# Performance work log

Hardware: AMD Instinct MI355X
Metric: run time of the kernel (lower is better)

Reference implementation:

```python
import jax, jax.numpy as jnp
import numpy as np

B, SECL, WORDL = 16, 8, 512
S = SECL * WORDL
H, E, V, NOOV = 256, 128, 50000, 32
EOS = 3
FSIZE = 2  # config.mode == 'train'


def setup_inputs() -> dict:
    key = jax.random.key(0)
    ks = jax.random.split(key, 24)
    g = lambda i, shape, s=0.02: jax.random.normal(ks[i], shape, jnp.float32) * s
    inp = jax.random.randint(ks[0], (B,), 0, V)
    inp = inp.at[:4].set(EOS)  # exercise focus-update branch
    h = g(1, (B, H), 0.1)
    c = g(2, (B, H), 0.1)
    enc_outputs = g(3, (B, S, 2 * H), 1.0)
    enc_feature = g(4, (B, S, 2 * H), 0.1)
    enc_sec_output = g(5, (B, SECL, 2 * H), 1.0)
    enc_mask = jnp.ones((B, S), jnp.float32)
    sec_mask = jnp.ones((B, SECL), jnp.float32)
    prev_context = g(6, (B, 2 * H), 0.1)
    zeros_oov = jnp.zeros((B, NOOV), jnp.float32)
    enc_input_oov = jax.random.randint(ks[7], (B, S), 0, V + NOOV)
    coverage = jnp.zeros((B, S), jnp.float32)
    # sparse nonneg focus distribution over sections (guaranteed >=1 nonzero/row)
    u = jax.random.uniform(ks[8], (B, SECL))
    f = u * (u > 0.5)
    fb = jax.nn.one_hot(jnp.argmax(u, axis=1), SECL)
    f = jnp.where(f.sum(1, keepdims=True) > 0, f, fb)
    focus = f / f.sum(1, keepdims=True)
    params = dict(
        embedding=g(9, (V, E)),
        W_comb=g(10, (E, 2 * H + E)), b_comb=jnp.zeros((E,), jnp.float32),
        W_ih=g(11, (4 * H, E)), W_hh=g(12, (4 * H, H)),
        b_ih=jnp.zeros((4 * H,), jnp.float32), b_hh=jnp.zeros((4 * H,), jnp.float32),
        W_d=g(13, (2 * H, 2 * H)), b_d=jnp.zeros((2 * H,), jnp.float32),
        W_feat=g(14, (2 * H, 2 * H)), v_sec=g(15, (2 * H,)),
        W_dec=g(16, (2 * H, 2 * H)), b_dec=jnp.zeros((2 * H,), jnp.float32),
        w_cov=g(17, (2 * H,)), v_att=g(18, (2 * H,)),
        W_pgen=g(19, (1, 4 * H + E)), b_pgen=jnp.zeros((1,), jnp.float32),
        W_out=g(20, (V, 3 * H)), b_out=g(21, (V,)),
    )
    return dict(inp=inp, h=h, c=c, enc_outputs=enc_outputs, enc_feature=enc_feature,
                enc_sec_output=enc_sec_output, enc_mask=enc_mask, sec_mask=sec_mask,
                prev_context=prev_context, zeros_oov=zeros_oov, enc_input_oov=enc_input_oov,
                coverage=coverage, focus=focus, **params)


def _focus_update(focus, sad):
    # rem_mask: positions from the first nonzero of focus onward
    fz = jnp.cumprod((focus == 0).astype(sad.dtype), axis=1)
    rem_mask = (fz == 0).astype(sad.dtype)
    focus_index = jnp.sum(fz, axis=1).astype(jnp.int32)  # index of first nonzero
    focus_mask = jax.nn.one_hot(focus_index, SECL, dtype=sad.dtype)
    rem_ex = rem_mask - focus_mask
    focus_beta = sad * focus_mask
    rem_beta = sad * rem_ex
    max_rem_beta = rem_beta.max(axis=1)
    max_rem_ind = jnp.argmax(rem_beta, axis=1)
    compare = (focus_beta.max(axis=1) * 2 > max_rem_beta).astype(sad.dtype)[:, None]
    # train branch
    src = (max_rem_beta != 0).astype(sad.dtype)[:, None]
    max_rem_mask = jax.nn.one_hot(max_rem_ind, SECL, dtype=sad.dtype) * src
    cp2 = jnp.cumprod((max_rem_mask == 0).astype(sad.dtype), axis=1)
    after = (cp2 == 0).astype(sad.dtype) - max_rem_mask
    amb = sad * after
    mam_mask = (jax.nn.one_hot(jnp.argmax(amb, axis=1), SECL, dtype=sad.dtype)
                * (amb.max(axis=1) != 0).astype(sad.dtype)[:, None])
    case_f = focus_beta + sad * max_rem_mask
    case_r = sad * (max_rem_mask + mam_mask)
    fu = compare * case_f + (1 - compare) * case_r
    return fu / fu.sum(1, keepdims=True)


def reference(inp, h, c, enc_outputs, enc_feature, enc_sec_output, enc_mask, sec_mask,
              prev_context, zeros_oov, enc_input_oov, coverage, focus,
              embedding, W_comb, b_comb, W_ih, W_hh, b_ih, b_hh,
              W_d, b_d, W_feat, v_sec, W_dec, b_dec, w_cov, v_att,
              W_pgen, b_pgen, W_out, b_out):
    inp_is_eos = (inp == EOS).astype(jnp.float32)[:, None]  # [B,1] -> bcast over secL
    emb = embedding[inp]  # [B,E]
    x = jnp.concatenate([prev_context, emb], axis=1) @ W_comb.T + b_comb  # [B,E]
    # single LSTM step (torch gate order i,f,g,o)
    gates = x @ W_ih.T + b_ih + h @ W_hh.T + b_hh
    gi_, gf_, gg_, go_ = jnp.split(gates, 4, axis=1)
    c_new = jax.nn.sigmoid(gf_) * c + jax.nn.sigmoid(gi_) * jnp.tanh(gg_)
    h_new = jax.nn.sigmoid(go_) * jnp.tanh(c_new)
    dec_state = jnp.concatenate([h_new, c_new], axis=1)  # [B,2H]
    # section attention
    feat = enc_sec_output @ W_feat.T  # [B,secL,2H]
    d = dec_state @ W_d.T + b_d
    sc = jnp.tanh(feat + d[:, None, :]) @ v_sec  # [B,secL]
    sad = jax.nn.softmax(sc, axis=1) * sec_mask
    sad = sad / sad.sum(1, keepdims=True)
    # hard-attention focus update (only where input was EOS)
    fu = _focus_update(focus, sad)
    focus = inp_is_eos * fu + (1 - inp_is_eos) * focus
    # word attention with coverage
    dfeat = dec_state @ W_dec.T + b_dec
    att = enc_feature + dfeat[:, None, :] + coverage[:, :, None] * w_cov[None, None, :]
    score = jnp.tanh(att) @ v_att  # [B,S]
    score3 = score.reshape(B, SECL, WORDL)
    topk_focus, gidx = jax.lax.top_k(focus, FSIZE)  # [B,FSIZE]
    bidx = jnp.arange(B)[:, None]
    score_g = score3[bidx, gidx].reshape(B, FSIZE * WORDL)
    mask_g = enc_mask.reshape(B, SECL, WORDL)[bidx, gidx].reshape(B, FSIZE * WORDL)
    af = jax.nn.softmax(score_g, axis=1) * mask_g
    af = af / af.sum(1, keepdims=True)
    af = topk_focus[:, :, None] * af.reshape(B, FSIZE, WORDL)
    attn = jnp.zeros((B, SECL, WORDL), af.dtype).at[bidx, gidx].set(af).reshape(B, S)
    attn = attn / attn.sum(1, keepdims=True)
    context = jnp.einsum('bs,bsd->bd', attn, enc_outputs)  # [B,2H]
    coverage = coverage + attn
    # pointer-generator
    p_gen = jax.nn.sigmoid(jnp.concatenate([context, dec_state, x], axis=1) @ W_pgen.T + b_pgen)
    logits = jnp.concatenate([h_new, context], axis=1) @ W_out.T + b_out
    vocab_dist = jax.nn.softmax(logits, axis=1)
    vext = jnp.concatenate([p_gen * vocab_dist, zeros_oov], axis=1)  # [B,V+NOOV]
    final = vext.at[bidx, enc_input_oov].add((1 - p_gen) * attn)
    return final, h_new, c_new, context, attn, coverage, focus, sad
```

## Files before the change

kernel.cpp:

```cpp
#include <hip/hip_runtime.h>
#include <math.h>

#define NB 16
#define SECL 8
#define WORDL 512
#define SS 4096
#define HH 256
#define EE 128
#define VV 50000
#define NOOV 32
#define VO 50032
#define EOS_ID 3
#define H2 512
#define KOUT 768
#define NCH 13
#define CHSZ 4096

#define OFF_FINAL 0
#define OFF_H    800512
#define OFF_C    804608
#define OFF_CTX  808704
#define OFF_ATTN 816896
#define OFF_COV  882432
#define OFF_FOC  947968
#define OFF_SAD  948096

#define WX     0
#define WD     2048
#define WDF    10240
#define WSC    18432
#define WGI    18560
#define WTF    18592
#define WSG    18624
#define WPART  35008
#define WPG    166080
#define WPM    166096
#define WPS    166304
#define WLG    166512

__device__ __forceinline__ float sigm(float x){ return 1.f/(1.f+__expf(-x)); }
__device__ __forceinline__ float tfast(float x){
  float ax = fabsf(x);
  float e  = __expf(-2.f*ax);
  float t  = (1.f-e)/(1.f+e);
  return x < 0.f ? -t : t;
}
__device__ __forceinline__ float dot4(float acc, float4 a, float4 b){
  acc = fmaf(a.x,b.x,acc); acc = fmaf(a.y,b.y,acc);
  acc = fmaf(a.z,b.z,acc); acc = fmaf(a.w,b.w,acc);
  return acc;
}
__device__ __forceinline__ float dot2(float acc, float2 a, float2 b){
  acc = fmaf(a.x,b.x,acc); acc = fmaf(a.y,b.y,acc);
  return acc;
}
__device__ __forceinline__ float mergep(float a, float b, int k, int lane){
  float send = (lane & k) ? a : b;
  float recv = __shfl_xor(send, k);
  return (lane & k) ? b + recv : a + recv;
}
__device__ __forceinline__ float reduce8(float acc[8], int lane){
  float m0 = mergep(acc[0], acc[1], 1, lane);
  float m1 = mergep(acc[2], acc[3], 1, lane);
  float m2 = mergep(acc[4], acc[5], 1, lane);
  float m3 = mergep(acc[6], acc[7], 1, lane);
  float n0 = mergep(m0, m1, 2, lane);
  float n1 = mergep(m2, m3, 2, lane);
  float p  = mergep(n0, n1, 4, lane);
  p += __shfl_xor(p, 8);
  p += __shfl_xor(p, 16);
  p += __shfl_xor(p, 32);
  return p;
}

__global__ void __launch_bounds__(256)
k_x(const int* __restrict__ inp, const float* __restrict__ pc,
    const float* __restrict__ emb, const float* __restrict__ Wc,
    const float* __restrict__ bc, float* __restrict__ ws){
  int lane = threadIdx.x & 63;
  int gw = blockIdx.x*4 + (threadIdx.x >> 6);
  int bg = gw & 1, e = gw >> 1;
  float4 z = {0,0,0,0};
  float4 i0[8], i1[8], i2[8];
  #pragma unroll
  for(int j=0;j<8;j++){
    int b = bg*8 + j;
    i0[j] = *(const float4*)(pc + b*H2 + lane*4);
    i1[j] = *(const float4*)(pc + b*H2 + 256 + lane*4);
    i2[j] = (lane < 32) ? *(const float4*)(emb + (size_t)inp[b]*EE + lane*4) : z;
  }
  const float* wr = Wc + (size_t)e*(H2+EE);
  float4 w0 = *(const float4*)(wr + lane*4);
  float4 w1 = *(const float4*)(wr + 256 + lane*4);
  float4 w2 = (lane < 32) ? *(const float4*)(wr + 512 + lane*4) : z;
  float acc[8];
  #pragma unroll
  for(int j=0;j<8;j++){
    float a = dot4(0.f, w0, i0[j]);
    a = dot4(a, w1, i1[j]);
    a = dot4(a, w2, i2[j]);
    acc[j] = a;
  }
  float p = reduce8(acc, lane);
  if(lane < 8) ws[WX + (bg*8+lane)*EE + e] = p + bc[e];
}

__global__ void __launch_bounds__(256)
k_gates(const float* __restrict__ h, const float* __restrict__ c,
        const float* __restrict__ Wih, const float* __restrict__ Whh,
        const float* __restrict__ bih, const float* __restrict__ bhh,
        const float* __restrict__ ws, float* __restrict__ out){
  __shared__ float g_lds[4][8];
  int lane = threadIdx.x & 63;
  int wv   = threadIdx.x >> 6;
  int j  = blockIdx.x >> 1;
  int bg = blockIdx.x & 1;
  float2 xb[8]; float4 hb[8];
  #pragma unroll
  for(int q=0;q<8;q++){
    int b = bg*8 + q;
    xb[q] = *(const float2*)(ws + WX + b*EE + lane*2);
    hb[q] = *(const float4*)(h + b*HH + lane*4);
  }
  int r = wv*HH + j;
  float2 wx = *(const float2*)(Wih + (size_t)r*EE + lane*2);
  float4 wh = *(const float4*)(Whh + (size_t)r*HH + lane*4);
  float acc[8];
  #pragma unroll
  for(int q=0;q<8;q++)
    acc[q] = dot4(dot2(0.f, wx, xb[q]), wh, hb[q]);
  float p = reduce8(acc, lane);
  if(lane < 8) g_lds[wv][lane] = p + bih[r] + bhh[r];
  __syncthreads();
  if(threadIdx.x < 8){
    int b = bg*8 + threadIdx.x;
    float g0 = g_lds[0][threadIdx.x], g1 = g_lds[1][threadIdx.x];
    float g2 = g_lds[2][threadIdx.x], g3 = g_lds[3][threadIdx.x];
    float cn = sigm(g1)*c[b*HH + j] + sigm(g0)*tfast(g2);
    float hn = sigm(g3)*tfast(cn);
    out[OFF_H + b*HH + j] = hn;
    out[OFF_C + b*HH + j] = cn;
  }
}

__global__ void __launch_bounds__(256)
k_dd(const float* __restrict__ Wd, const float* __restrict__ bd,
     const float* __restrict__ Wdec, const float* __restrict__ bdec,
     const float* __restrict__ out, float* __restrict__ ws){
  int lane = threadIdx.x & 63;
  int gw = blockIdx.x*4 + (threadIdx.x >> 6);
  int bg = gw & 1, sel = (gw >> 1) & 1, j = gw >> 2;
  float4 d0[8], d1[8];
  #pragma unroll
  for(int q=0;q<8;q++){
    int b = bg*8 + q;
    d0[q] = *(const float4*)(out + OFF_H + b*HH + lane*4);
    d1[q] = *(const float4*)(out + OFF_C + b*HH + lane*4);
  }
  const float* wr = (sel ? Wdec : Wd) + (size_t)j*H2;
  float4 w0 = *(const float4*)(wr + lane*4);
  float4 w1 = *(const float4*)(wr + 256 + lane*4);
  float acc[8];
  #pragma unroll
  for(int q=0;q<8;q++)
    acc[q] = dot4(dot4(0.f, w0, d0[q]), w1, d1[q]);
  float p = reduce8(acc, lane);
  if(lane < 8) ws[(sel ? WDF : WD) + (bg*8+lane)*H2 + j] = p + (sel ? bdec : bd)[j];
}

__global__ void __launch_bounds__(256)
k_sec(const float* __restrict__ eso, const float* __restrict__ Wf,
      const float* __restrict__ vsec, float* __restrict__ ws){
  __shared__ float red[4];
  int lane = threadIdx.x & 63;
  int wv   = threadIdx.x >> 6;
  int bl = blockIdx.x; int b = bl >> 3;
  const float* ep = eso + (size_t)bl*H2;
  float4 es0 = *(const float4*)(ep + lane*4);
  float4 es1 = *(const float4*)(ep + 256 + lane*4);
  const float* dp = ws + WD + b*H2;
  float local = 0.f;
  for(int t=0;t<16;t++){
    int j0 = wv*8 + t*32;
    float acc[8];
    #pragma unroll
    for(int jj=0;jj<8;jj++){
      const float* wr = Wf + (size_t)(j0+jj)*H2;
      float4 w0 = *(const float4*)(wr + lane*4);
      float4 w1 = *(const float4*)(wr + 256 + lane*4);
      acc[jj] = dot4(dot4(0.f, w0, es0), w1, es1);
    }
    float p = reduce8(acc, lane);
    if(lane < 8){
      int j = j0 + lane;
      local += tfast(p + dp[j]) * vsec[j];
    }
  }
  local += __shfl_xor(local, 1);
  local += __shfl_xor(local, 2);
  local += __shfl_xor(local, 4);
  if(lane == 0) red[wv] = local;
  __syncthreads();
  if(threadIdx.x == 0) ws[WSC + bl] = red[0]+red[1]+red[2]+red[3];
}

__global__ void k_focus(const int* __restrict__ inp, const float* __restrict__ smask,
                        const float* __restrict__ focus_in, float* __restrict__ ws,
                        float* __restrict__ out){
  int b = threadIdx.x;
  if(b >= NB) return;
  float sc[SECL], sad[SECL], f[SECL];
  float mx = -1e30f;
  for(int l=0;l<SECL;l++){ sc[l] = ws[WSC + b*SECL + l]; mx = fmaxf(mx, sc[l]); }
  float sum = 0.f;
  for(int l=0;l<SECL;l++){ sad[l] = __expf(sc[l]-mx); sum += sad[l]; }
  float s2 = 0.f;
  for(int l=0;l<SECL;l++){ sad[l] = sad[l]/sum * smask[b*SECL+l]; s2 += sad[l]; }
  for(int l=0;l<SECL;l++){ sad[l] /= s2; out[OFF_SAD + b*SECL + l] = sad[l]; }
  for(int l=0;l<SECL;l++) f[l] = focus_in[b*SECL+l];
  int fi = SECL;
  for(int l=0;l<SECL;l++){ if(f[l] != 0.f){ fi = l; break; } }
  float rem[SECL];
  for(int l=0;l<SECL;l++) rem[l] = (l > fi) ? sad[l] : 0.f;
  float mrb = rem[0]; int mri = 0;
  for(int l=1;l<SECL;l++){ if(rem[l] > mrb){ mrb = rem[l]; mri = l; } }
  float fbm = (fi < SECL) ? sad[fi] : 0.f;
  int cmp = (fbm*2.f > mrb);
  int src = (mrb != 0.f);
  float amb[SECL];
  for(int l=0;l<SECL;l++) amb[l] = (src && l > mri) ? sad[l] : 0.f;
  float am = amb[0]; int ai = 0;
  for(int l=1;l<SECL;l++){ if(amb[l] > am){ am = amb[l]; ai = l; } }
  float fu[SECL]; float fs = 0.f;
  for(int l=0;l<SECL;l++){
    float mrm = (src && l == mri) ? 1.f : 0.f;
    float mam = ((am != 0.f) && l == ai) ? 1.f : 0.f;
    float cf = ((l==fi) ? sad[l] : 0.f) + sad[l]*mrm;
    float cr = sad[l]*(mrm + mam);
    fu[l] = cmp ? cf : cr;
    fs += fu[l];
  }
  float eos = (inp[b] == EOS_ID) ? 1.f : 0.f;
  float fo[SECL];
  for(int l=0;l<SECL;l++){
    fo[l] = eos*(fu[l]/fs) + (1.f-eos)*f[l];
    out[OFF_FOC + b*SECL + l] = fo[l];
  }
  float v1 = fo[0]; int i1 = 0;
  for(int l=1;l<SECL;l++){ if(fo[l] > v1){ v1 = fo[l]; i1 = l; } }
  float v2 = -1e30f; int i2 = 0;
  for(int l=0;l<SECL;l++){ if(l != i1 && fo[l] > v2){ v2 = fo[l]; i2 = l; } }
  ((int*)ws)[WGI + b*2]     = i1;
  ((int*)ws)[WGI + b*2 + 1] = i2;
  ws[WTF + b*2]     = v1;
  ws[WTF + b*2 + 1] = v2;
}

__global__ void k_score(const float* __restrict__ ef, const float* __restrict__ cov,
                        const float* __restrict__ wcov, const float* __restrict__ vatt,
                        float* __restrict__ ws){
  int lane = threadIdx.x & 63;
  int o = blockIdx.x*4 + (threadIdx.x >> 6);
  int b = o >> 10, fidx = (o >> 9) & 1, w = o & 511;
  int g = ((const int*)ws)[WGI + b*2 + fidx];
  int s = g*WORDL + w;
  const float* e  = ef + ((size_t)(b*SS + s))*H2;
  const float* df = ws + WDF + b*H2;
  float cv = cov[b*SS + s];
  int j = lane*4;
  float local = 0.f;
  #pragma unroll
  for(int half=0; half<2; half++){
    int jj = j + half*256;
    float4 a  = *(const float4*)(e+jj);
    float4 d4 = *(const float4*)(df+jj);
    float4 wc = *(const float4*)(wcov+jj);
    float4 va = *(const float4*)(vatt+jj);
    local += tfast(a.x + d4.x + cv*wc.x)*va.x;
    local += tfast(a.y + d4.y + cv*wc.y)*va.y;
    local += tfast(a.z + d4.z + cv*wc.z)*va.z;
    local += tfast(a.w + d4.w + cv*wc.w)*va.w;
  }
  for(int off=32; off>0; off>>=1) local += __shfl_xor(local, off);
  if(lane == 0) ws[WSG + o] = local;
}

__global__ void k_af(const float* __restrict__ emask, const float* __restrict__ cov,
                     float* __restrict__ ws, float* __restrict__ out){
  __shared__ float es[1024];
  __shared__ float red[256];
  int b = blockIdx.x, tid = threadIdx.x;
  int g0 = ((int*)ws)[WGI+b*2], g1 = ((int*)ws)[WGI+b*2+1];
  float tf0 = ws[WTF+b*2], tf1 = ws[WTF+b*2+1];
  float lm = -1e30f;
  for(int i=tid;i<1024;i+=256) lm = fmaxf(lm, ws[WSG + b*1024 + i]);
  red[tid] = lm; __syncthreads();
  for(int off=128; off; off>>=1){
    if(tid < off) red[tid] = fmaxf(red[tid], red[tid+off]);
    __syncthreads();
  }
  float mx = red[0]; __syncthreads();
  float ls0 = 0.f, ls1 = 0.f;
  for(int i=tid;i<1024;i+=256){
    int fidx = i >> 9, w = i & 511;
    int g = fidx ? g1 : g0;
    float m = emask[b*SS + g*WORDL + w];
    float ev = __expf(ws[WSG + b*1024 + i] - mx)*m;
    es[i] = ev;
    if(fidx) ls1 += ev; else ls0 += ev;
  }
  red[tid] = ls0; __syncthreads();
  for(int off=128; off; off>>=1){ if(tid<off) red[tid]+=red[tid+off]; __syncthreads(); }
  float sum0 = red[0]; __syncthreads();
  red[tid] = ls1; __syncthreads();
  for(int off=128; off; off>>=1){ if(tid<off) red[tid]+=red[tid+off]; __syncthreads(); }
  float sum1 = red[0]; __syncthreads();
  float inv = 1.f/(tf0*sum0 + tf1*sum1);
  for(int s=tid;s<SS;s+=256){
    int sec = s >> 9, w = s & 511;
    float a = 0.f;
    if(sec == g0)      a = tf0*es[w]*inv;
    else if(sec == g1) a = tf1*es[512+w]*inv;
    out[OFF_ATTN + b*SS + s] = a;
    out[OFF_COV  + b*SS + s] = cov[b*SS+s] + a;
  }
}

__global__ void k_ctxp(const float* __restrict__ eo, const float* __restrict__ out,
                       float* __restrict__ ws){
  int blk = blockIdx.x; int b = blk >> 4, ch = blk & 15;
  int d = threadIdx.x;
  int g0 = ((const int*)ws)[WGI + b*2];
  int g1 = ((const int*)ws)[WGI + b*2 + 1];
  float a0 = 0.f, a1 = 0.f;
  #pragma unroll 4
  for(int p = ch*64; p < ch*64 + 64; p++){
    int s = ((p >> 9) ? g1 : g0)*WORDL + (p & 511);
    float a = out[OFF_ATTN + b*SS + s];
    const float* ep = eo + ((size_t)(b*SS + s))*H2;
    a0 = fmaf(a, ep[d],       a0);
    a1 = fmaf(a, ep[d+256],   a1);
  }
  ws[WPART + (size_t)blk*H2 + d]       = a0;
  ws[WPART + (size_t)blk*H2 + d + 256] = a1;
}

__global__ void k_ctx(const float* __restrict__ Wp, const float* __restrict__ bp,
                      float* __restrict__ ws, float* __restrict__ out){
  __shared__ float red[256];
  int b = blockIdx.x, tid = threadIdx.x;
  float c0 = 0.f, c1 = 0.f;
  for(int ch=0; ch<16; ch++){
    c0 += ws[WPART + (size_t)(b*16+ch)*H2 + tid];
    c1 += ws[WPART + (size_t)(b*16+ch)*H2 + tid + 256];
  }
  out[OFF_CTX + b*H2 + tid]       = c0;
  out[OFF_CTX + b*H2 + tid + 256] = c1;
  float hn = out[OFF_H + b*HH + tid];
  float cn = out[OFF_C + b*HH + tid];
  float pv = c0*Wp[tid] + c1*Wp[tid+256] + hn*Wp[512+tid] + cn*Wp[768+tid];
  if(tid < EE) pv = fmaf(ws[WX + b*EE + tid], Wp[1024+tid], pv);
  red[tid] = pv; __syncthreads();
  for(int off=128; off; off>>=1){ if(tid<off) red[tid]+=red[tid+off]; __syncthreads(); }
  if(tid == 0) ws[WPG + b] = sigm(red[0] + bp[0]);
}

__global__ void __launch_bounds__(256,3)
k_logits(const float* __restrict__ Wout, const float* __restrict__ bout,
         const float* __restrict__ out, float* __restrict__ ws){
  int lane = threadIdx.x & 63;
  int wv   = threadIdx.x >> 6;
  int bg   = wv & 1;
  int rh   = wv >> 1;
  float4 hb0[8], hb1[8], hb2[8];
  #pragma unroll
  for(int j=0;j<8;j++){
    int b = bg*8 + j;
    hb0[j] = *(const float4*)(out + OFF_H   + b*HH + lane*4);
    hb1[j] = *(const float4*)(out + OFF_CTX + b*H2 + lane*4);
    hb2[j] = *(const float4*)(out + OFF_CTX + b*H2 + 256 + lane*4);
  }
  int v = blockIdx.x*32 + rh;
  int vc = v < VV ? v : VV-1;
  const float* wp = Wout + (size_t)vc*KOUT + lane*4;
  float4 a0 = *(const float4*)(wp);
  float4 a1 = *(const float4*)(wp+256);
  float4 a2 = *(const float4*)(wp+512);
  #pragma unroll 2
  for(int r=0;r<16;r++){
    int vn = v + 2;
    int vnc = vn < VV ? vn : VV-1;
    const float* np = Wout + (size_t)vnc*KOUT + lane*4;
    float4 n0 = *(const float4*)(np);
    float4 n1 = *(const float4*)(np+256);
    float4 n2 = *(const float4*)(np+512);
    float acc[8];
    #pragma unroll
    for(int j=0;j<8;j++){
      float a = dot4(0.f, a0, hb0[j]);
      a = dot4(a, a1, hb1[j]);
      a = dot4(a, a2, hb2[j]);
      acc[j] = a;
    }
    float p = reduce8(acc, lane);
    if(v < VV && lane < 8)
      ws[WLG + (size_t)(bg*8+lane)*VV + v] = p + bout[v];
    a0 = n0; a1 = n1; a2 = n2;
    v = vn;
  }
}

__global__ void k_vms(float* __restrict__ ws){
  __shared__ float rm[256], rs[256];
  int blk = blockIdx.x; int b = blk/NCH, ch = blk%NCH;
  int tid = threadIdx.x;
  int v0 = ch*CHSZ; int v1 = v0+CHSZ; if(v1 > VV) v1 = VV;
  float mt = -1e30f, st = 0.f;
  for(int v=v0+tid; v<v1; v+=256){
    float x = ws[WLG + (size_t)b*VV + v];
    if(x > mt){ st = st*__expf(mt - x) + 1.f; mt = x; }
    else       st += __expf(x - mt);
  }
  rm[tid] = mt; rs[tid] = st; __syncthreads();
  for(int off=128; off; off>>=1){
    if(tid < off){
      float ma = rm[tid], mb = rm[tid+off];
      float M = fmaxf(ma, mb);
      rs[tid] = rs[tid]*__expf(ma-M) + rs[tid+off]*__expf(mb-M);
      rm[tid] = M;
    }
    __syncthreads();
  }
  if(tid == 0){ ws[WPM + blk] = rm[0]; ws[WPS + blk] = rs[0]; }
}

__global__ void k_final(const float* __restrict__ zoov, float* __restrict__ ws,
                        float* __restrict__ out){
  int blk = blockIdx.x; int b = blk/NCH, ch = blk%NCH;
  float mx = -1e30f, sm = 0.f;
  for(int i=0;i<NCH;i++){ mx = fmaxf(mx, ws[WPM + b*NCH + i]); }
  for(int i=0;i<NCH;i++){ sm += ws[WPS + b*NCH + i]*__expf(ws[WPM + b*NCH + i] - mx); }
  float scale = ws[WPG + b] / sm;
  int v0 = ch*CHSZ; int v1 = v0+CHSZ; if(v1 > VO) v1 = VO;
  for(int v=v0+threadIdx.x; v<v1; v+=256){
    float r;
    if(v < VV) r = scale*__expf(ws[WLG + (size_t)b*VV + v] - mx);
    else       r = zoov[b*NOOV + v - VV];
    out[OFF_FINAL + (size_t)b*VO + v] = r;
  }
}

__global__ void k_scatter(const int* __restrict__ oov, const float* __restrict__ ws,
                          float* __restrict__ out){
  int blk = blockIdx.x; int b = blk >> 4;
  int s = (blk & 15)*256 + threadIdx.x;
  float a = out[OFF_ATTN + b*SS + s];
  if(a != 0.f){
    float w = (1.f - ws[WPG + b])*a;
    atomicAdd(out + OFF_FINAL + (size_t)b*VO + oov[b*SS + s], w);
  }
}

extern "C" void kernel_launch(void* const* d_in, const int* in_sizes, int n_in,
                              void* d_out, int out_size, void* d_ws, size_t ws_size,
                              hipStream_t stream){
  const int*   inp   = (const int*)  d_in[0];
  const float* h     = (const float*)d_in[1];
  const float* c     = (const float*)d_in[2];
  const float* eo    = (const float*)d_in[3];
  const float* efeat = (const float*)d_in[4];
  const float* eso   = (const float*)d_in[5];
  const float* emask = (const float*)d_in[6];
  const float* smask = (const float*)d_in[7];
  const float* pctx  = (const float*)d_in[8];
  const float* zoov  = (const float*)d_in[9];
  const int*   oov   = (const int*)  d_in[10];
  const float* cov   = (const float*)d_in[11];
  const float* foc   = (const float*)d_in[12];
  const float* emb   = (const float*)d_in[13];
  const float* Wc    = (const float*)d_in[14];
  const float* bc    = (const float*)d_in[15];
  const float* Wih   = (const float*)d_in[16];
  const float* Whh   = (const float*)d_in[17];
  const float* bih   = (const float*)d_in[18];
  const float* bhh   = (const float*)d_in[19];
  const float* Wd    = (const float*)d_in[20];
  const float* bd    = (const float*)d_in[21];
  const float* Wf    = (const float*)d_in[22];
  const float* vsec  = (const float*)d_in[23];
  const float* Wdec  = (const float*)d_in[24];
  const float* bdec  = (const float*)d_in[25];
  const float* wcov  = (const float*)d_in[26];
  const float* vatt  = (const float*)d_in[27];
  const float* Wp    = (const float*)d_in[28];
  const float* bp    = (const float*)d_in[29];
  const float* Wout  = (const float*)d_in[30];
  const float* bout  = (const float*)d_in[31];
  float* out = (float*)d_out;
  float* ws  = (float*)d_ws;

  k_x      <<<64,   256, 0, stream>>>(inp, pctx, emb, Wc, bc, ws);
  k_gates  <<<512,  256, 0, stream>>>(h, c, Wih, Whh, bih, bhh, ws, out);
  k_dd     <<<512,  256, 0, stream>>>(Wd, bd, Wdec, bdec, out, ws);
  k_sec    <<<128,  256, 0, stream>>>(eso, Wf, vsec, ws);
  k_focus  <<<1,     64, 0, stream>>>(inp, smask, foc, ws, out);
  k_score  <<<4096, 256, 0, stream>>>(efeat, cov, wcov, vatt, ws);
  k_af     <<<16,   256, 0, stream>>>(emask, cov, ws, out);
  k_ctxp   <<<256,  256, 0, stream>>>(eo, out, ws);
  k_ctx    <<<16,   256, 0, stream>>>(Wp, bp, ws, out);
  k_logits <<<1563, 256, 0, stream>>>(Wout, bout, out, ws);
  k_vms    <<<208,  256, 0, stream>>>(ws);
  k_final  <<<208,  256, 0, stream>>>(zoov, ws, out);
  k_scatter<<<256,  256, 0, stream>>>(oov, ws, out);
}
```

Baseline: 139.5 us.

## Restructure logits GEMV to stage W_out tiles and activations in LDS

```diff
diff --git a/kernel.cpp b/kernel.cpp
--- a/kernel.cpp
+++ b/kernel.cpp
@@ -72,6 +72,7 @@
   p += __shfl_xor(p, 32);
   return p;
 }
+
 
 __global__ void __launch_bounds__(256)
 k_x(const int* __restrict__ inp, const float* __restrict__ pc,
@@ -256,6 +257,7 @@
   ws[WTF + b*2 + 1] = v2;
 }
 
+
 __global__ void k_score(const float* __restrict__ ef, const float* __restrict__ cov,
                         const float* __restrict__ wcov, const float* __restrict__ vatt,
                         float* __restrict__ ws){
@@ -365,50 +367,72 @@
   if(tid == 0) ws[WPG + b] = sigm(red[0] + bp[0]);
 }
 
-__global__ void __launch_bounds__(256,3)
+#define LROWS 16
+#define PADW 49
+#define PADH 17
+__global__ void __launch_bounds__(256,2)
 k_logits(const float* __restrict__ Wout, const float* __restrict__ bout,
          const float* __restrict__ out, float* __restrict__ ws){
-  int lane = threadIdx.x & 63;
-  int wv   = threadIdx.x >> 6;
-  int bg   = wv & 1;
-  int rh   = wv >> 1;
-  float4 hb0[8], hb1[8], hb2[8];
-  #pragma unroll
-  for(int j=0;j<8;j++){
-    int b = bg*8 + j;
-    hb0[j] = *(const float4*)(out + OFF_H   + b*HH + lane*4);
-    hb1[j] = *(const float4*)(out + OFF_CTX + b*H2 + lane*4);
-    hb2[j] = *(const float4*)(out + OFF_CTX + b*H2 + 256 + lane*4);
-  }
-  int v = blockIdx.x*32 + rh;
-  int vc = v < VV ? v : VV-1;
-  const float* wp = Wout + (size_t)vc*KOUT + lane*4;
-  float4 a0 = *(const float4*)(wp);
-  float4 a1 = *(const float4*)(wp+256);
-  float4 a2 = *(const float4*)(wp+512);
-  #pragma unroll 2
-  for(int r=0;r<16;r++){
-    int vn = v + 2;
-    int vnc = vn < VV ? vn : VV-1;
-    const float* np = Wout + (size_t)vnc*KOUT + lane*4;
-    float4 n0 = *(const float4*)(np);
-    float4 n1 = *(const float4*)(np+256);
-    float4 n2 = *(const float4*)(np+512);
-    float acc[8];
+  __shared__ float4 hbT[192*PADH];
+  __shared__ float4 Wq[2][LROWS*PADW];
+  int tid = threadIdx.x;
+  int v0 = blockIdx.x*LROWS;
+  {
+    int b = tid >> 4, kcol = tid & 15;
+    const float* hsrc = out + OFF_H   + b*HH;
+    const float* csrc = out + OFF_CTX + b*H2;
     #pragma unroll
-    for(int j=0;j<8;j++){
-      float a = dot4(0.f, a0, hb0[j]);
-      a = dot4(a, a1, hb1[j]);
-      a = dot4(a, a2, hb2[j]);
-      acc[j] = a;
-    }
-    float p = reduce8(acc, lane);
-    if(v < VV && lane < 8)
-      ws[WLG + (size_t)(bg*8+lane)*VV + v] = p + bout[v];
-    a0 = n0; a1 = n1; a2 = n2;
-    v = vn;
-  }
-}
+    for(int j=0;j<12;j++){
+      int k4 = kcol + 16*j;
+      float4 v = (k4 < 64) ? *(const float4*)(hsrc + k4*4)
+                           : *(const float4*)(csrc + (k4-64)*4);
+      hbT[k4*PADH + b] = v;
+    }
+  }
+  int r = tid >> 4, cc = tid & 15;
+  {
+    const float* wr = Wout + (size_t)(v0+r)*KOUT;
+    #pragma unroll
+    for(int j=0;j<3;j++){
+      int k4 = cc + 16*j;
+      Wq[0][r*PADW + k4] = *(const float4*)(wr + k4*4);
+    }
+  }
+  __syncthreads();
+  int b = tid & 15, vloc = tid >> 4;
+  int buf = 0;
+  float a0=0,a1=0,a2=0,a3=0;
+  #pragma unroll
+  for(int q=0;q<4;q++){
+    float4 p0,p1,p2;
+    if(q<3){
+      const float* wr = Wout + (size_t)(v0+r)*KOUT + (q+1)*192;
+      p0 = *(const float4*)(wr + cc*4);
+      p1 = *(const float4*)(wr + (cc+16)*4);
+      p2 = *(const float4*)(wr + (cc+32)*4);
+    }
+    const float4* wrow = &Wq[buf][vloc*PADW];
+    const float4* hcol = &hbT[q*48*PADH + b];
+    #pragma unroll
+    for(int kk=0;kk<48;kk+=4){
+      a0 = dot4(a0, wrow[kk],   hcol[(kk  )*PADH]);
+      a1 = dot4(a1, wrow[kk+1], hcol[(kk+1)*PADH]);
+      a2 = dot4(a2, wrow[kk+2], hcol[(kk+2)*PADH]);
+      a3 = dot4(a3, wrow[kk+3], hcol[(kk+3)*PADH]);
+    }
+    if(q<3){
+      Wq[buf^1][r*PADW + cc]      = p0;
+      Wq[buf^1][r*PADW + cc + 16] = p1;
+      Wq[buf^1][r*PADW + cc + 32] = p2;
+      __syncthreads();
+      buf ^= 1;
+    }
+  }
+  float acc = (a0+a1)+(a2+a3);
+  int v = v0 + vloc;
+  ws[WLG + (size_t)b*VV + v] = acc + bout[v];
+}
+
 
 __global__ void k_vms(float* __restrict__ ws){
   __shared__ float rm[256], rs[256];
@@ -508,7 +532,7 @@
   k_af     <<<16,   256, 0, stream>>>(emask, cov, ws, out);
   k_ctxp   <<<256,  256, 0, stream>>>(eo, out, ws);
   k_ctx    <<<16,   256, 0, stream>>>(Wp, bp, ws, out);
-  k_logits <<<1563, 256, 0, stream>>>(Wout, bout, out, ws);
+  k_logits <<<3125, 256, 0, stream>>>(Wout, bout, out, ws);
   k_vms    <<<208,  256, 0, stream>>>(ws);
   k_final  <<<208,  256, 0, stream>>>(zoov, ws, out);
   k_scatter<<<256,  256, 0, stream>>>(oov, ws, out);
```

New measurement: 155.4 us. 11.4% more time.

## Make logits kernel grid-stride with 768 blocks and two-deep row prefetch

Applied to the files above, without the earlier changes.

```diff
diff --git a/kernel.cpp b/kernel.cpp
--- a/kernel.cpp
+++ b/kernel.cpp
@@ -72,6 +72,7 @@
   p += __shfl_xor(p, 32);
   return p;
 }
+
 
 __global__ void __launch_bounds__(256)
 k_x(const int* __restrict__ inp, const float* __restrict__ pc,
@@ -256,6 +257,7 @@
   ws[WTF + b*2 + 1] = v2;
 }
 
+
 __global__ void k_score(const float* __restrict__ ef, const float* __restrict__ cov,
                         const float* __restrict__ wcov, const float* __restrict__ vatt,
                         float* __restrict__ ws){
@@ -365,6 +367,9 @@
   if(tid == 0) ws[WPG + b] = sigm(red[0] + bp[0]);
 }
 
+#define LG_NBLK  768
+#define LG_STRIDE (LG_NBLK*2)
+#define LG_ITERS 33
 __global__ void __launch_bounds__(256,3)
 k_logits(const float* __restrict__ Wout, const float* __restrict__ bout,
          const float* __restrict__ out, float* __restrict__ ws){
@@ -380,35 +385,42 @@
     hb1[j] = *(const float4*)(out + OFF_CTX + b*H2 + lane*4);
     hb2[j] = *(const float4*)(out + OFF_CTX + b*H2 + 256 + lane*4);
   }
-  int v = blockIdx.x*32 + rh;
-  int vc = v < VV ? v : VV-1;
-  const float* wp = Wout + (size_t)vc*KOUT + lane*4;
-  float4 a0 = *(const float4*)(wp);
-  float4 a1 = *(const float4*)(wp+256);
-  float4 a2 = *(const float4*)(wp+512);
-  #pragma unroll 2
-  for(int r=0;r<16;r++){
-    int vn = v + 2;
-    int vnc = vn < VV ? vn : VV-1;
-    const float* np = Wout + (size_t)vnc*KOUT + lane*4;
-    float4 n0 = *(const float4*)(np);
-    float4 n1 = *(const float4*)(np+256);
-    float4 n2 = *(const float4*)(np+512);
+  int vbase = blockIdx.x*2 + rh;
+  const float* p0 = Wout + (size_t)vbase*KOUT + lane*4;
+  float4 A0 = *(const float4*)(p0);
+  float4 A1 = *(const float4*)(p0+256);
+  float4 A2 = *(const float4*)(p0+512);
+  int v1c = vbase + LG_STRIDE; if(v1c >= VV) v1c = VV-1;
+  const float* p1 = Wout + (size_t)v1c*KOUT + lane*4;
+  float4 B0 = *(const float4*)(p1);
+  float4 B1 = *(const float4*)(p1+256);
+  float4 B2 = *(const float4*)(p1+512);
+  for(int j=0;j<LG_ITERS;j++){
+    int v = vbase + j*LG_STRIDE;
+    float4 C0=B0, C1=B1, C2=B2;
+    if(j < LG_ITERS-2){
+      int vn = v + 2*LG_STRIDE; if(vn >= VV) vn = VV-1;
+      const float* np = Wout + (size_t)vn*KOUT + lane*4;
+      C0 = *(const float4*)(np);
+      C1 = *(const float4*)(np+256);
+      C2 = *(const float4*)(np+512);
+    }
     float acc[8];
     #pragma unroll
-    for(int j=0;j<8;j++){
-      float a = dot4(0.f, a0, hb0[j]);
-      a = dot4(a, a1, hb1[j]);
-      a = dot4(a, a2, hb2[j]);
-      acc[j] = a;
+    for(int q=0;q<8;q++){
+      float a = dot4(0.f, A0, hb0[q]);
+      a = dot4(a, A1, hb1[q]);
+      a = dot4(a, A2, hb2[q]);
+      acc[q] = a;
     }
     float p = reduce8(acc, lane);
     if(v < VV && lane < 8)
       ws[WLG + (size_t)(bg*8+lane)*VV + v] = p + bout[v];
-    a0 = n0; a1 = n1; a2 = n2;
-    v = vn;
-  }
-}
+    A0=B0; A1=B1; A2=B2;
+    B0=C0; B1=C1; B2=C2;
+  }
+}
+
 
 __global__ void k_vms(float* __restrict__ ws){
   __shared__ float rm[256], rs[256];
@@ -499,17 +511,17 @@
   float* out = (float*)d_out;
   float* ws  = (float*)d_ws;
 
-  k_x      <<<64,   256, 0, stream>>>(inp, pctx, emb, Wc, bc, ws);
-  k_gates  <<<512,  256, 0, stream>>>(h, c, Wih, Whh, bih, bhh, ws, out);
-  k_dd     <<<512,  256, 0, stream>>>(Wd, bd, Wdec, bdec, out, ws);
-  k_sec    <<<128,  256, 0, stream>>>(eso, Wf, vsec, ws);
-  k_focus  <<<1,     64, 0, stream>>>(inp, smask, foc, ws, out);
-  k_score  <<<4096, 256, 0, stream>>>(efeat, cov, wcov, vatt, ws);
-  k_af     <<<16,   256, 0, stream>>>(emask, cov, ws, out);
-  k_ctxp   <<<256,  256, 0, stream>>>(eo, out, ws);
-  k_ctx    <<<16,   256, 0, stream>>>(Wp, bp, ws, out);
-  k_logits <<<1563, 256, 0, stream>>>(Wout, bout, out, ws);
-  k_vms    <<<208,  256, 0, stream>>>(ws);
-  k_final  <<<208,  256, 0, stream>>>(zoov, ws, out);
-  k_scatter<<<256,  256, 0, stream>>>(oov, ws, out);
-}
+  k_x      <<<64,      256, 0, stream>>>(inp, pctx, emb, Wc, bc, ws);
+  k_gates  <<<512,     256, 0, stream>>>(h, c, Wih, Whh, bih, bhh, ws, out);
+  k_dd     <<<512,     256, 0, stream>>>(Wd, bd, Wdec, bdec, out, ws);
+  k_sec    <<<128,     256, 0, stream>>>(eso, Wf, vsec, ws);
+  k_focus  <<<1,        64, 0, stream>>>(inp, smask, foc, ws, out);
+  k_score  <<<4096,    256, 0, stream>>>(efeat, cov, wcov, vatt, ws);
+  k_af     <<<16,      256, 0, stream>>>(emask, cov, ws, out);
+  k_ctxp   <<<256,     256, 0, stream>>>(eo, out, ws);
+  k_ctx    <<<16,      256, 0, stream>>>(Wp, bp, ws, out);
+  k_logits <<<LG_NBLK, 256, 0, stream>>>(Wout, bout, out, ws);
+  k_vms    <<<208,     256, 0, stream>>>(ws);
+  k_final  <<<208,     256, 0, stream>>>(zoov, ws, out);
+  k_scatter<<<256,     256, 0, stream>>>(oov, ws, out);
+}
```

Result: faster. 131.1 us (-6.0%).
